# Kernel optimization log

Measured on AMD Instinct MI355X. Metric: run time of the kernel, lower is better.

Reference implementation:

```python
import jax, jax.numpy as jnp
import numpy as np

DIM = 192
HEADS = 6
HD = DIM // HEADS
WS = 7
R = 128  # low-rank projected sequence length
N_FULL = 3136  # 56*56
B = 32


def setup_inputs() -> dict:
    key = jax.random.key(0)
    ks = jax.random.split(key, 9)
    s = 0.02
    return {
        "x": jax.random.normal(ks[0], (2048, WS * WS, DIM), dtype=jnp.float32),
        "qkv_w": jax.random.normal(ks[1], (3 * DIM, DIM), dtype=jnp.float32) * s,
        "qkv_b": jax.random.normal(ks[2], (3 * DIM,), dtype=jnp.float32) * s,
        "E_w": jax.random.normal(ks[3], (R, N_FULL), dtype=jnp.float32) * s,
        "E_b": jax.random.normal(ks[4], (R,), dtype=jnp.float32) * s,
        "F_w": jax.random.normal(ks[5], (R, N_FULL), dtype=jnp.float32) * s,
        "F_b": jax.random.normal(ks[6], (R,), dtype=jnp.float32) * s,
        "proj_w": jax.random.normal(ks[7], (DIM, DIM), dtype=jnp.float32) * s,
        "proj_b": jax.random.normal(ks[8], (DIM,), dtype=jnp.float32) * s,
        "h": 56,
        "w": 56,
    }


def reference(x, qkv_w, qkv_b, E_w, E_b, F_w, F_b, proj_w, proj_b, h, w):
    C = x.shape[-1]
    # window_reverse: (nW*B, ws*ws, C) -> (B, H*W, C)
    xw = x.reshape(-1, WS, WS, C)
    b = xw.shape[0] // ((h // WS) * (w // WS))
    xm = xw.reshape(b, h // WS, w // WS, WS, WS, C)
    xm = xm.transpose(0, 1, 3, 2, 4, 5).reshape(b, h * w, C)
    n = h * w
    scale = 1.0 / np.sqrt(HD)

    qkv = (xm @ qkv_w.T + qkv_b).reshape(b, n, 3, HEADS, HD)
    qkv = qkv.transpose(2, 0, 3, 1, 4)  # (3, b, heads, n, hd)
    q, k, v = qkv[0] * scale, qkv[1], qkv[2]

    # Linformer low-rank projection along sequence: (b,h,n,d) -> (b,h,R,d)
    k_low = jnp.einsum('bhnd,kn->bhkd', k, E_w) + E_b[None, None, :, None]
    v_low = jnp.einsum('bhnd,kn->bhkd', v, F_w) + F_b[None, None, :, None]

    attn = jnp.einsum('bhnd,bhkd->bhnk', q, k_low)  # (b, heads, n, R)
    attn = jax.nn.softmax(attn, axis=-1)

    out = jnp.einsum('bhnk,bhkd->bhnd', attn, v_low)
    out = out.transpose(0, 2, 1, 3).reshape(b, n, C)
    out = out @ proj_w.T + proj_b
    return out
```

## Files before the change

kernel.cpp:

```cpp
#include <hip/hip_runtime.h>

typedef __bf16 bf16;
typedef bf16 bf16x8 __attribute__((ext_vector_type(8)));
typedef bf16 bf16x4 __attribute__((ext_vector_type(4)));
typedef float f32x4 __attribute__((ext_vector_type(4)));

#define MFMA16(a,b,c) __builtin_amdgcn_mfma_f32_16x16x32_bf16(a,b,c,0,0,0)

#define NSEQ 3136
#define CDIM 192

__device__ inline bf16x8 cvt8(float4 a, float4 b) {
  bf16x8 r;
  r[0]=(bf16)a.x; r[1]=(bf16)a.y; r[2]=(bf16)a.z; r[3]=(bf16)a.w;
  r[4]=(bf16)b.x; r[5]=(bf16)b.y; r[6]=(bf16)b.z; r[7]=(bf16)b.w;
  return r;
}

__device__ inline bf16x4 cvt4(float4 a) {
  bf16x4 r;
  r[0]=(bf16)a.x; r[1]=(bf16)a.y; r[2]=(bf16)a.z; r[3]=(bf16)a.w;
  return r;
}

__global__ void k_prep(const float* __restrict__ qkv_w, const float* __restrict__ E_w,
                       const float* __restrict__ F_w, const float* __restrict__ proj_w,
                       bf16* __restrict__ qkvw, bf16* __restrict__ EF, bf16* __restrict__ projw,
                       float* __restrict__ rowsums) {
  if (blockIdx.x < 256) {
    __shared__ float red[4];
    int row = blockIdx.x;
    const float* src = (row < 128) ? (E_w + (long)row * NSEQ) : (F_w + (long)(row - 128) * NSEQ);
    float s = 0.f;
    for (int i = threadIdx.x; i < 784; i += 256) {
      float4 f = *(const float4*)(src + i * 4);
      s += f.x + f.y + f.z + f.w;
    }
    for (int off = 32; off; off >>= 1) s += __shfl_xor(s, off);
    if ((threadIdx.x & 63) == 0) red[threadIdx.x >> 6] = s;
    __syncthreads();
    if (threadIdx.x == 0) rowsums[row] = red[0] + red[1] + red[2] + red[3];
  } else {
    int i4 = (blockIdx.x - 256) * blockDim.x + threadIdx.x;
    const int tot4 = 950272 / 4;
    const int stride = 480 * 256;
    for (; i4 < tot4; i4 += stride) {
      int i = i4 * 4;
      float4 f;
      bf16* dst;
      if (i < 110592)      { f = *(const float4*)(qkv_w + i);            dst = qkvw + i; }
      else if (i < 512000) { f = *(const float4*)(E_w + (i - 110592));   dst = EF + (i - 110592); }
      else if (i < 913408) { f = *(const float4*)(F_w + (i - 512000));   dst = EF + (i - 110592); }
      else                 { f = *(const float4*)(proj_w + (i - 913408)); dst = projw + (i - 913408); }
      *(bf16x4*)dst = cvt4(f);
    }
  }
}

__launch_bounds__(256, 4)
__global__ void k_xTq(const float* __restrict__ x, const bf16* __restrict__ qkvw,
                      const float* __restrict__ qkv_b, bf16* __restrict__ xmT,
                      bf16* __restrict__ q) {
  __shared__ bf16 tile[64][196];
  int blk = blockIdx.x;
  int b = blk / 49, n0 = (blk % 49) * 64;
  int tid = threadIdx.x;
  int wid = tid >> 6, lane = tid & 63;
  int lrow = lane & 15, hi = lane >> 4, lk = hi * 8;
  for (int e = tid; e < 3072; e += 256) {
    int row = e / 48, c4 = e % 48;
    int n = n0 + row;
    int r = n / 56, cc = n % 56;
    long srcrow = (long)(b * 64 + (r / 7) * 8 + (cc / 7)) * 49 + (r % 7) * 7 + (cc % 7);
    float4 f = *(const float4*)(x + srcrow * 192 + c4 * 4);
    *(bf16x4*)&tile[row][c4 * 4] = cvt4(f);
  }
  __syncthreads();
  f32x4 zero = {0.f, 0.f, 0.f, 0.f};
  f32x4 acc[12];
  for (int j = 0; j < 12; j++) acc[j] = zero;
  const bf16* wq = qkvw + (long)lrow * 192 + lk;
  for (int ks = 0; ks < 6; ks++) {
    bf16x8 af = *(bf16x8*)&tile[wid * 16 + lrow][ks * 32 + lk];
    const bf16* wp = wq + ks * 32;
    for (int j = 0; j < 12; j++) {
      bf16x8 bv = *(const bf16x8*)(wp + (long)j * 16 * 192);
      acc[j] = MFMA16(af, bv, acc[j]);
    }
  }
  for (int e = tid; e < 1536; e += 256) {
    int c = e >> 3, k = e & 7;
    bf16x8 v;
    for (int jj = 0; jj < 8; jj++) v[jj] = tile[k * 8 + jj][c];
    *(bf16x8*)(xmT + ((long)b * 192 + c) * NSEQ + n0 + k * 8) = v;
  }
  __syncthreads();
  const float scale = 0.17677669529663687f;
  for (int j = 0; j < 12; j++) {
    int c = 16 * j + lrow;
    float bias = qkv_b[c];
    for (int rr = 0; rr < 4; rr++)
      tile[wid * 16 + hi * 4 + rr][c] = (bf16)((acc[j][rr] + bias) * scale);
  }
  __syncthreads();
  for (int e = tid; e < 1536; e += 256) {
    int row = e / 24, ch = e % 24;
    bf16x4 lo = *(bf16x4*)&tile[row][ch * 8];
    bf16x4 hh = *(bf16x4*)&tile[row][ch * 8 + 4];
    bf16x8 v;
    v[0]=lo[0]; v[1]=lo[1]; v[2]=lo[2]; v[3]=lo[3];
    v[4]=hh[0]; v[5]=hh[1]; v[6]=hh[2]; v[7]=hh[3];
    *(bf16x8*)(q + ((long)b * NSEQ + n0 + row) * 192 + ch * 8) = v;
  }
}

__launch_bounds__(512)
__global__ void k_xlow(const bf16* __restrict__ EF, const bf16* __restrict__ xmT,
                       float* __restrict__ partial) {
  __shared__ bf16 As[256][72];
  __shared__ bf16 Bs[192][72];
  int idx = blockIdx.x;
  int s = idx % 7, b = idx / 7;
  int kbase = s * 448;
  int tid = threadIdx.x;
  int wid = tid >> 6, lane = tid & 63;
  int wm = wid >> 2, wn = wid & 3;
  int lrow = lane & 15, hi = lane >> 4, lk = hi * 8;
  f32x4 zero = {0.f, 0.f, 0.f, 0.f};
  f32x4 acc[8][3];
  for (int i = 0; i < 8; i++) for (int j = 0; j < 3; j++) acc[i][j] = zero;
  for (int k0 = 0; k0 < 448; k0 += 64) {
    for (int i = 0; i < 4; i++) {
      int unit = i * 512 + tid;
      int row = unit >> 3, koff = (unit & 7) * 8;
      *(bf16x8*)&As[row][koff] = *(const bf16x8*)(EF + (long)row * NSEQ + kbase + k0 + koff);
    }
    for (int i = 0; i < 3; i++) {
      int unit = i * 512 + tid;
      int row = unit >> 3, koff = (unit & 7) * 8;
      *(bf16x8*)&Bs[row][koff] = *(const bf16x8*)(xmT + ((long)b * 192 + row) * NSEQ + kbase + k0 + koff);
    }
    __syncthreads();
    for (int ks = 0; ks < 2; ks++) {
      bf16x8 af[8], bfv[3];
      for (int i = 0; i < 8; i++) af[i]  = *(bf16x8*)&As[wm * 128 + 16 * i + lrow][ks * 32 + lk];
      for (int j = 0; j < 3; j++) bfv[j] = *(bf16x8*)&Bs[wn * 48 + 16 * j + lrow][ks * 32 + lk];
      for (int i = 0; i < 8; i++) for (int j = 0; j < 3; j++) acc[i][j] = MFMA16(af[i], bfv[j], acc[i][j]);
    }
    __syncthreads();
  }
  float* P = partial + (long)idx * 49152;
  for (int i = 0; i < 8; i++) for (int j = 0; j < 3; j++) for (int rr = 0; rr < 4; rr++) {
    int rl = wm * 128 + 16 * i + hi * 4 + rr;
    int cl = wn * 48 + 16 * j + lrow;
    P[rl * 192 + cl] = acc[i][j][rr];
  }
}

__global__ void k_reduce(const float* __restrict__ partial, bf16* __restrict__ el_fl) {
  int blk = blockIdx.x;
  int b = blk / 48, ch = blk % 48;
  long e = (long)ch * 1024 + threadIdx.x * 4;
  const float* P = partial + (long)b * 7 * 49152 + e;
  float4 sum = {0.f, 0.f, 0.f, 0.f};
  for (int s = 0; s < 7; s++) {
    float4 f = *(const float4*)(P + (long)s * 49152);
    sum.x += f.x; sum.y += f.y; sum.z += f.z; sum.w += f.w;
  }
  *(bf16x4*)(el_fl + (long)b * 49152 + e) = cvt4(sum);
}

__launch_bounds__(256)
__global__ void k_lowproj(const bf16* __restrict__ el_fl, const bf16* __restrict__ qkvw,
                          const float* __restrict__ qkv_b, const float* __restrict__ E_b,
                          const float* __restrict__ F_b, const float* __restrict__ rowsums,
                          bf16* __restrict__ k_lowH, bf16* __restrict__ v_lowT) {
  __shared__ bf16 As[64][200];
  __shared__ bf16 Bs[64][200];
  int idx = blockIdx.x;
  int b = idx / 12, rem = idx % 12;
  int type = rem / 6; rem %= 6;
  int bm, bn;
  if (type == 0) { bm = rem / 3; bn = rem % 3; }
  else           { bm = rem / 2; bn = rem % 2; }
  int m0 = bm * 64, n0 = bn * 64;
  int tid = threadIdx.x;
  int wid = tid >> 6, lane = tid & 63;
  int wm = wid >> 1, wn = wid & 1;
  int lrow = lane & 15, lk = (lane >> 4) * 8;
  int srow = tid >> 2, skoff = (tid & 3) * 16;
  const bf16* Ap; const bf16* Bp;
  if (type == 0) {
    Ap = el_fl + ((long)b * 256 + m0 + srow) * 192 + skoff;
    Bp = qkvw + (long)(192 + n0 + srow) * 192 + skoff;
  } else {
    Ap = qkvw + (long)(384 + m0 + srow) * 192 + skoff;
    Bp = el_fl + ((long)b * 256 + 128 + n0 + srow) * 192 + skoff;
  }
  for (int kk = 0; kk < 192; kk += 64) {
    *(bf16x8*)&As[srow][kk + skoff]     = *(const bf16x8*)(Ap + kk);
    *(bf16x8*)&As[srow][kk + skoff + 8] = *(const bf16x8*)(Ap + kk + 8);
    *(bf16x8*)&Bs[srow][kk + skoff]     = *(const bf16x8*)(Bp + kk);
    *(bf16x8*)&Bs[srow][kk + skoff + 8] = *(const bf16x8*)(Bp + kk + 8);
  }
  __syncthreads();
  f32x4 zero = {0.f, 0.f, 0.f, 0.f};
  f32x4 acc[2][2];
  for (int i = 0; i < 2; i++) for (int j = 0; j < 2; j++) acc[i][j] = zero;
  for (int ks = 0; ks < 6; ks++) {
    bf16x8 af[2], bfv[2];
    for (int i = 0; i < 2; i++) af[i]  = *(bf16x8*)&As[wm * 32 + 16 * i + lrow][ks * 32 + lk];
    for (int j = 0; j < 2; j++) bfv[j] = *(bf16x8*)&Bs[wn * 32 + 16 * j + lrow][ks * 32 + lk];
    for (int i = 0; i < 2; i++) for (int j = 0; j < 2; j++) acc[i][j] = MFMA16(af[i], bfv[j], acc[i][j]);
  }
  if (type == 0) {
    for (int i = 0; i < 2; i++) for (int j = 0; j < 2; j++) for (int rr = 0; rr < 4; rr++) {
      int kr = m0 + wm * 32 + 16 * i + (lane >> 4) * 4 + rr;
      int c = n0 + wn * 32 + 16 * j + lrow;
      float v = acc[i][j][rr] + rowsums[kr] * qkv_b[192 + c] + E_b[kr];
      k_lowH[(((long)b * 6 + (c >> 5)) * 128 + kr) * 32 + (c & 31)] = (bf16)v;
    }
  } else {
    for (int i = 0; i < 2; i++) for (int j = 0; j < 2; j++) for (int rr = 0; rr < 4; rr++) {
      int c = m0 + wm * 32 + 16 * i + (lane >> 4) * 4 + rr;
      int kr = n0 + wn * 32 + 16 * j + lrow;
      float v = acc[i][j][rr] + rowsums[128 + kr] * qkv_b[384 + c] + F_b[kr];
      v_lowT[((long)b * 192 + c) * 128 + kr] = (bf16)v;
    }
  }
}

__launch_bounds__(256)
__global__ void k_attn(const bf16* __restrict__ q, const bf16* __restrict__ k_lowH,
                       const bf16* __restrict__ v_lowT, bf16* __restrict__ out_att) {
  __shared__ bf16 Ks[128][40];
  __shared__ bf16 Vs[32][136];
  __shared__ bf16 Ps[4][16][136];
  int idx = blockIdx.x;
  int nt = idx % 49, bh = idx / 49;
  int h = bh % 6, b = bh / 6;
  int n0 = nt * 64;
  int tid = threadIdx.x;
  int wid = tid >> 6, lane = tid & 63;
  int lrow = lane & 15, hi = lane >> 4, lk = hi * 8;
  {
    int row = tid >> 1, koff = (tid & 1) * 16;
    const bf16* src = k_lowH + (((long)b * 6 + h) * 128 + row) * 32 + koff;
    *(bf16x8*)&Ks[row][koff] = *(const bf16x8*)src;
    *(bf16x8*)&Ks[row][koff + 8] = *(const bf16x8*)(src + 8);
  }
  {
    int row = tid >> 3, koff = (tid & 7) * 16;
    const bf16* src = v_lowT + ((long)b * 192 + h * 32 + row) * 128 + koff;
    *(bf16x8*)&Vs[row][koff] = *(const bf16x8*)src;
    *(bf16x8*)&Vs[row][koff + 8] = *(const bf16x8*)(src + 8);
  }
  int nrow = n0 + wid * 16 + lrow;
  bf16x8 qf = *(const bf16x8*)(q + ((long)b * NSEQ + nrow) * 192 + h * 32 + lk);
  __syncthreads();
  f32x4 zero = {0.f, 0.f, 0.f, 0.f};
  f32x4 s[8];
  for (int f = 0; f < 8; f++) {
    bf16x8 kf = *(bf16x8*)&Ks[16 * f + lrow][lk];
    s[f] = MFMA16(kf, qf, zero);
  }
  float m = s[0][0];
  for (int f = 0; f < 8; f++) for (int rr = 0; rr < 4; rr++) m = fmaxf(m, s[f][rr]);
  m = fmaxf(m, __shfl_xor(m, 16));
  m = fmaxf(m, __shfl_xor(m, 32));
  float sum = 0.f;
  for (int f = 0; f < 8; f++) for (int rr = 0; rr < 4; rr++) {
    float p = __expf(s[f][rr] - m);
    s[f][rr] = p; sum += p;
  }
  sum += __shfl_xor(sum, 16);
  sum += __shfl_xor(sum, 32);
  float inv = 1.0f / sum;
  for (int f = 0; f < 8; f++) {
    bf16x4 pv;
    for (int rr = 0; rr < 4; rr++) pv[rr] = (bf16)(s[f][rr] * inv);
    *(bf16x4*)&Ps[wid][lrow][16 * f + hi * 4] = pv;
  }
  __syncthreads();
  f32x4 o[2];
  o[0] = zero; o[1] = zero;
  for (int ks = 0; ks < 4; ks++) {
    bf16x8 pf = *(bf16x8*)&Ps[wid][lrow][ks * 32 + lk];
    for (int j = 0; j < 2; j++) {
      bf16x8 vf = *(bf16x8*)&Vs[16 * j + lrow][ks * 32 + lk];
      o[j] = MFMA16(pf, vf, o[j]);
    }
  }
  for (int j = 0; j < 2; j++) for (int rr = 0; rr < 4; rr++) {
    int nn = n0 + wid * 16 + hi * 4 + rr;
    out_att[((long)b * NSEQ + nn) * 192 + h * 32 + 16 * j + lrow] = (bf16)o[j][rr];
  }
}

__launch_bounds__(256)
__global__ void k_proj(const bf16* __restrict__ oa, const bf16* __restrict__ projw,
                       const float* __restrict__ proj_b, float* __restrict__ out) {
  __shared__ bf16 As[128][104];
  __shared__ bf16 Bs[192][200];
  long g0 = (long)blockIdx.x * 128;
  int tid = threadIdx.x;
  int wid = tid >> 6, lane = tid & 63;
  int lrow = lane & 15, lk = (lane >> 4) * 8;
  {
    int koff = (tid & 3) * 48;
    for (int r0 = 0; r0 < 192; r0 += 64) {
      int row = r0 + (tid >> 2);
      const bf16* Bp = projw + (long)row * 192 + koff;
      for (int m = 0; m < 6; m++)
        *(bf16x8*)&Bs[row][koff + 8 * m] = *(const bf16x8*)(Bp + 8 * m);
    }
  }
  int arow = tid >> 1, half = tid & 1;
  const bf16* Ap = oa + (g0 + arow) * 192 + half * 48;
  f32x4 zero = {0.f, 0.f, 0.f, 0.f};
  f32x4 acc[2][12];
  for (int i = 0; i < 2; i++) for (int j = 0; j < 12; j++) acc[i][j] = zero;
  for (int k0 = 0; k0 < 192; k0 += 96) {
    for (int m = 0; m < 6; m++)
      *(bf16x8*)&As[arow][half * 48 + 8 * m] = *(const bf16x8*)(Ap + k0 + 8 * m);
    __syncthreads();
    for (int ks = 0; ks < 3; ks++) {
      bf16x8 af[2];
      for (int i = 0; i < 2; i++) af[i] = *(bf16x8*)&As[wid * 32 + 16 * i + lrow][ks * 32 + lk];
      for (int j = 0; j < 12; j++) {
        bf16x8 bv = *(bf16x8*)&Bs[16 * j + lrow][k0 + ks * 32 + lk];
        acc[0][j] = MFMA16(af[0], bv, acc[0][j]);
        acc[1][j] = MFMA16(af[1], bv, acc[1][j]);
      }
    }
    __syncthreads();
  }
  for (int i = 0; i < 2; i++) for (int j = 0; j < 12; j++) for (int rr = 0; rr < 4; rr++) {
    long grow = g0 + wid * 32 + 16 * i + (lane >> 4) * 4 + rr;
    int c = 16 * j + lrow;
    out[grow * 192 + c] = acc[i][j][rr] + proj_b[c];
  }
}

extern "C" void kernel_launch(void* const* d_in, const int* in_sizes, int n_in,
                              void* d_out, int out_size, void* d_ws, size_t ws_size,
                              hipStream_t stream) {
  const float* x      = (const float*)d_in[0];
  const float* qkv_w  = (const float*)d_in[1];
  const float* qkv_b  = (const float*)d_in[2];
  const float* E_w    = (const float*)d_in[3];
  const float* E_b    = (const float*)d_in[4];
  const float* F_w    = (const float*)d_in[5];
  const float* F_b    = (const float*)d_in[6];
  const float* proj_w = (const float*)d_in[7];
  const float* proj_b = (const float*)d_in[8];
  float* out = (float*)d_out;

  char* ws = (char*)d_ws;
  size_t off = 0;
  auto alloc = [&](size_t bytes) { char* p = ws + off; off += (bytes + 255) & ~(size_t)255; return p; };
  bf16* qkvw     = (bf16*)alloc((size_t)110592 * 2);
  bf16* EF       = (bf16*)alloc((size_t)802816 * 2);
  bf16* projw    = (bf16*)alloc((size_t)36864 * 2);
  float* rowsums = (float*)alloc((size_t)256 * 4);
  bf16* xmT      = (bf16*)alloc((size_t)32 * 192 * NSEQ * 2);
  bf16* q        = (bf16*)alloc((size_t)32 * NSEQ * 192 * 2);
  float* partial = (float*)alloc((size_t)224 * 49152 * 4);
  bf16* el_fl    = (bf16*)alloc((size_t)32 * 256 * 192 * 2);
  bf16* k_lowH   = (bf16*)alloc((size_t)32 * 6 * 128 * 32 * 2);
  bf16* v_lowT   = (bf16*)alloc((size_t)32 * 192 * 128 * 2);
  bf16* out_att  = xmT;

  k_prep<<<dim3(736), dim3(256), 0, stream>>>(qkv_w, E_w, F_w, proj_w, qkvw, EF, projw, rowsums);
  k_xTq<<<dim3(32 * 49), dim3(256), 0, stream>>>(x, qkvw, qkv_b, xmT, q);
  k_xlow<<<dim3(224), dim3(512), 0, stream>>>(EF, xmT, partial);
  k_reduce<<<dim3(1536), dim3(256), 0, stream>>>(partial, el_fl);
  k_lowproj<<<dim3(384), dim3(256), 0, stream>>>(el_fl, qkvw, qkv_b, E_b, F_b, rowsums, k_lowH, v_lowT);
  k_attn<<<dim3(32 * 6 * 49), dim3(256), 0, stream>>>(q, k_lowH, v_lowT, out_att);
  k_proj<<<dim3(784), dim3(256), 0, stream>>>(out_att, projw, proj_b, out);
}
```

Before: 315.5 us.

## Split xlow GEMM over M halves, restructure proj GEMM, prefetch weight fragments

k_xlow now splits the 256-row E/F dimension across two blocks, doubling the grid to 448 blocks and halving per-block accumulators and shared memory. This is meant to fill more compute units on the 256-CU device. k_proj is rewritten to use 64-row tiles and to read weight fragments straight from global/L2 instead of staging the full weight in LDS. k_xTq and k_proj now prefetch all 12 weight fragments per k-step in an unrolled loop, with launch bounds relaxed to 2 blocks per CU. The trade-off is higher register pressure and more redundant xmT reads in k_xlow.

```diff
diff --git a/kernel.cpp b/kernel.cpp
--- a/kernel.cpp
+++ b/kernel.cpp
@@ -57,7 +57,7 @@
   }
 }
 
-__launch_bounds__(256, 4)
+__launch_bounds__(256, 2)
 __global__ void k_xTq(const float* __restrict__ x, const bf16* __restrict__ qkvw,
                       const float* __restrict__ qkv_b, bf16* __restrict__ xmT,
                       bf16* __restrict__ q) {
@@ -80,13 +80,14 @@
   f32x4 acc[12];
   for (int j = 0; j < 12; j++) acc[j] = zero;
   const bf16* wq = qkvw + (long)lrow * 192 + lk;
+  #pragma unroll
   for (int ks = 0; ks < 6; ks++) {
+    bf16x8 bv[12];
+    #pragma unroll
+    for (int j = 0; j < 12; j++) bv[j] = *(const bf16x8*)(wq + j * 3072 + ks * 32);
     bf16x8 af = *(bf16x8*)&tile[wid * 16 + lrow][ks * 32 + lk];
-    const bf16* wp = wq + ks * 32;
-    for (int j = 0; j < 12; j++) {
-      bf16x8 bv = *(const bf16x8*)(wp + (long)j * 16 * 192);
-      acc[j] = MFMA16(af, bv, acc[j]);
-    }
+    #pragma unroll
+    for (int j = 0; j < 12; j++) acc[j] = MFMA16(af, bv[j], acc[j]);
   }
   for (int e = tid; e < 1536; e += 256) {
     int c = e >> 3, k = e & 7;
@@ -117,23 +118,26 @@
 __launch_bounds__(512)
 __global__ void k_xlow(const bf16* __restrict__ EF, const bf16* __restrict__ xmT,
                        float* __restrict__ partial) {
-  __shared__ bf16 As[256][72];
+  __shared__ bf16 As[128][72];
   __shared__ bf16 Bs[192][72];
   int idx = blockIdx.x;
-  int s = idx % 7, b = idx / 7;
+  int mh = idx & 1;
+  int s = (idx >> 1) % 7;
+  int b = idx / 14;
   int kbase = s * 448;
+  int m0 = mh * 128;
   int tid = threadIdx.x;
   int wid = tid >> 6, lane = tid & 63;
   int wm = wid >> 2, wn = wid & 3;
   int lrow = lane & 15, hi = lane >> 4, lk = hi * 8;
   f32x4 zero = {0.f, 0.f, 0.f, 0.f};
-  f32x4 acc[8][3];
-  for (int i = 0; i < 8; i++) for (int j = 0; j < 3; j++) acc[i][j] = zero;
+  f32x4 acc[4][3];
+  for (int i = 0; i < 4; i++) for (int j = 0; j < 3; j++) acc[i][j] = zero;
   for (int k0 = 0; k0 < 448; k0 += 64) {
-    for (int i = 0; i < 4; i++) {
+    for (int i = 0; i < 2; i++) {
       int unit = i * 512 + tid;
       int row = unit >> 3, koff = (unit & 7) * 8;
-      *(bf16x8*)&As[row][koff] = *(const bf16x8*)(EF + (long)row * NSEQ + kbase + k0 + koff);
+      *(bf16x8*)&As[row][koff] = *(const bf16x8*)(EF + (long)(m0 + row) * NSEQ + kbase + k0 + koff);
     }
     for (int i = 0; i < 3; i++) {
       int unit = i * 512 + tid;
@@ -142,16 +146,16 @@
     }
     __syncthreads();
     for (int ks = 0; ks < 2; ks++) {
-      bf16x8 af[8], bfv[3];
-      for (int i = 0; i < 8; i++) af[i]  = *(bf16x8*)&As[wm * 128 + 16 * i + lrow][ks * 32 + lk];
+      bf16x8 af[4], bfv[3];
+      for (int i = 0; i < 4; i++) af[i]  = *(bf16x8*)&As[wm * 64 + 16 * i + lrow][ks * 32 + lk];
       for (int j = 0; j < 3; j++) bfv[j] = *(bf16x8*)&Bs[wn * 48 + 16 * j + lrow][ks * 32 + lk];
-      for (int i = 0; i < 8; i++) for (int j = 0; j < 3; j++) acc[i][j] = MFMA16(af[i], bfv[j], acc[i][j]);
+      for (int i = 0; i < 4; i++) for (int j = 0; j < 3; j++) acc[i][j] = MFMA16(af[i], bfv[j], acc[i][j]);
     }
     __syncthreads();
   }
-  float* P = partial + (long)idx * 49152;
-  for (int i = 0; i < 8; i++) for (int j = 0; j < 3; j++) for (int rr = 0; rr < 4; rr++) {
-    int rl = wm * 128 + 16 * i + hi * 4 + rr;
+  float* P = partial + (long)(b * 7 + s) * 49152 + (long)m0 * 192;
+  for (int i = 0; i < 4; i++) for (int j = 0; j < 3; j++) for (int rr = 0; rr < 4; rr++) {
+    int rl = wm * 64 + 16 * i + hi * 4 + rr;
     int cl = wn * 48 + 16 * j + lrow;
     P[rl * 192 + cl] = acc[i][j][rr];
   }
@@ -297,48 +301,39 @@
   }
 }
 
-__launch_bounds__(256)
+__launch_bounds__(256, 2)
 __global__ void k_proj(const bf16* __restrict__ oa, const bf16* __restrict__ projw,
                        const float* __restrict__ proj_b, float* __restrict__ out) {
-  __shared__ bf16 As[128][104];
-  __shared__ bf16 Bs[192][200];
-  long g0 = (long)blockIdx.x * 128;
-  int tid = threadIdx.x;
-  int wid = tid >> 6, lane = tid & 63;
-  int lrow = lane & 15, lk = (lane >> 4) * 8;
-  {
-    int koff = (tid & 3) * 48;
-    for (int r0 = 0; r0 < 192; r0 += 64) {
-      int row = r0 + (tid >> 2);
-      const bf16* Bp = projw + (long)row * 192 + koff;
-      for (int m = 0; m < 6; m++)
-        *(bf16x8*)&Bs[row][koff + 8 * m] = *(const bf16x8*)(Bp + 8 * m);
-    }
-  }
-  int arow = tid >> 1, half = tid & 1;
-  const bf16* Ap = oa + (g0 + arow) * 192 + half * 48;
-  f32x4 zero = {0.f, 0.f, 0.f, 0.f};
-  f32x4 acc[2][12];
-  for (int i = 0; i < 2; i++) for (int j = 0; j < 12; j++) acc[i][j] = zero;
-  for (int k0 = 0; k0 < 192; k0 += 96) {
-    for (int m = 0; m < 6; m++)
-      *(bf16x8*)&As[arow][half * 48 + 8 * m] = *(const bf16x8*)(Ap + k0 + 8 * m);
-    __syncthreads();
-    for (int ks = 0; ks < 3; ks++) {
-      bf16x8 af[2];
-      for (int i = 0; i < 2; i++) af[i] = *(bf16x8*)&As[wid * 32 + 16 * i + lrow][ks * 32 + lk];
-      for (int j = 0; j < 12; j++) {
-        bf16x8 bv = *(bf16x8*)&Bs[16 * j + lrow][k0 + ks * 32 + lk];
-        acc[0][j] = MFMA16(af[0], bv, acc[0][j]);
-        acc[1][j] = MFMA16(af[1], bv, acc[1][j]);
-      }
-    }
-    __syncthreads();
-  }
-  for (int i = 0; i < 2; i++) for (int j = 0; j < 12; j++) for (int rr = 0; rr < 4; rr++) {
-    long grow = g0 + wid * 32 + 16 * i + (lane >> 4) * 4 + rr;
+  __shared__ bf16 As[64][200];
+  long g0 = (long)blockIdx.x * 64;
+  int tid = threadIdx.x;
+  int wid = tid >> 6, lane = tid & 63;
+  int lrow = lane & 15, hi = lane >> 4, lk = hi * 8;
+  for (int e = tid; e < 1536; e += 256) {
+    int row = e / 24, ch = e % 24;
+    *(bf16x8*)&As[row][ch * 8] = *(const bf16x8*)(oa + (g0 + row) * 192 + ch * 8);
+  }
+  __syncthreads();
+  f32x4 zero = {0.f, 0.f, 0.f, 0.f};
+  f32x4 acc[12];
+  for (int j = 0; j < 12; j++) acc[j] = zero;
+  const bf16* wb = projw + (long)lrow * 192 + lk;
+  #pragma unroll
+  for (int ks = 0; ks < 6; ks++) {
+    bf16x8 bv[12];
+    #pragma unroll
+    for (int j = 0; j < 12; j++) bv[j] = *(const bf16x8*)(wb + j * 3072 + ks * 32);
+    bf16x8 af = *(bf16x8*)&As[wid * 16 + lrow][ks * 32 + lk];
+    #pragma unroll
+    for (int j = 0; j < 12; j++) acc[j] = MFMA16(af, bv[j], acc[j]);
+  }
+  for (int j = 0; j < 12; j++) {
     int c = 16 * j + lrow;
-    out[grow * 192 + c] = acc[i][j][rr] + proj_b[c];
+    float pb = proj_b[c];
+    for (int rr = 0; rr < 4; rr++) {
+      long grow = g0 + wid * 16 + hi * 4 + rr;
+      out[grow * 192 + c] = acc[j][rr] + pb;
+    }
   }
 }
 
@@ -373,9 +368,9 @@
 
   k_prep<<<dim3(736), dim3(256), 0, stream>>>(qkv_w, E_w, F_w, proj_w, qkvw, EF, projw, rowsums);
   k_xTq<<<dim3(32 * 49), dim3(256), 0, stream>>>(x, qkvw, qkv_b, xmT, q);
-  k_xlow<<<dim3(224), dim3(512), 0, stream>>>(EF, xmT, partial);
+  k_xlow<<<dim3(448), dim3(512), 0, stream>>>(EF, xmT, partial);
   k_reduce<<<dim3(1536), dim3(256), 0, stream>>>(partial, el_fl);
   k_lowproj<<<dim3(384), dim3(256), 0, stream>>>(el_fl, qkvw, qkv_b, E_b, F_b, rowsums, k_lowH, v_lowT);
   k_attn<<<dim3(32 * 6 * 49), dim3(256), 0, stream>>>(q, k_lowH, v_lowT, out_att);
-  k_proj<<<dim3(784), dim3(256), 0, stream>>>(out_att, projw, proj_b, out);
-}
+  k_proj<<<dim3(32 * 49), dim3(256), 0, stream>>>(out_att, projw, proj_b, out);
+}
```

Result: slower. 345.3 us (+9.4%).
